# Kernel optimization log

Measured on AMD Instinct MI355X. Metric: run time of the kernel, lower is better.

## Reference

```python
import jax, jax.numpy as jnp
import numpy as np

B, T, E, H, A = 64, 1024, 512, 512, 512  # batch, src_len, enc_dim, hidden, attention_dim
D_IN = 512                                # decoder input embedding dim; cell input = D_IN + E


def setup_inputs() -> dict:
    key = jax.random.key(0)
    ks = jax.random.split(key, 10)
    s = 0.05  # small init to keep tanh/sigmoid unsaturated
    return {
        "inputs":  jax.random.normal(ks[0], (B, D_IN), jnp.float32),
        "states":  jax.random.normal(ks[1], (B, H), jnp.float32),
        "encoded": jax.random.normal(ks[2], (B, T, E), jnp.float32),
        "W_enc":   jax.random.normal(ks[3], (E, A), jnp.float32) * s,
        "W_state": jax.random.normal(ks[4], (H, A), jnp.float32) * s,
        "v":       jax.random.normal(ks[5], (A,), jnp.float32) * s,
        "W_ih":    jax.random.normal(ks[6], (3 * H, D_IN + E), jnp.float32) * s,
        "W_hh":    jax.random.normal(ks[7], (3 * H, H), jnp.float32) * s,
        "b_ih":    jnp.zeros((3 * H,), jnp.float32),
        "b_hh":    jnp.zeros((3 * H,), jnp.float32),
    }


def reference(inputs, states, encoded, W_enc, W_state, v, W_ih, W_hh, b_ih, b_hh):
    # --- Bahdanau additive attention (one decoder step) ---
    enc_proj = jnp.einsum("bte,ea->bta", encoded, W_enc)      # setup_memory projection
    st_proj = states @ W_state                                  # [B,A]
    scores = jnp.tanh(enc_proj + st_proj[:, None, :]) @ v       # [B,T]
    weights = jax.nn.softmax(scores, axis=-1)                   # [B,T]
    context = jnp.einsum("bt,bte->be", weights, encoded)       # [B,E]

    # --- GRU cell step on concat(inputs, context) (torch.nn.GRUCell math) ---
    x = jnp.concatenate([inputs, context], axis=-1)             # [B, D_IN+E]
    gi = x @ W_ih.T + b_ih                                      # [B, 3H]
    gh = states @ W_hh.T + b_hh                                 # [B, 3H]
    i_r, i_z, i_n = jnp.split(gi, 3, axis=-1)
    h_r, h_z, h_n = jnp.split(gh, 3, axis=-1)
    r = jax.nn.sigmoid(i_r + h_r)
    z = jax.nn.sigmoid(i_z + h_z)
    n = jnp.tanh(i_n + r * h_n)
    return (1.0 - z) * n + z * states                           # [B,H]
```

## Files before the change

kernel.cpp:

```cpp
#include <hip/hip_runtime.h>
#include <hip/hip_bf16.h>

#define BN   64
#define TN   1024
#define EN   512
#define AN   512
#define HN   512
#define G3H  1536

typedef __bf16 bf16x8 __attribute__((ext_vector_type(8)));
typedef __bf16 bf16x4 __attribute__((ext_vector_type(4)));
typedef float  f32x8  __attribute__((ext_vector_type(8)));
typedef float  f32x4  __attribute__((ext_vector_type(4)));
typedef unsigned int uint4v __attribute__((ext_vector_type(4)));

__device__ __forceinline__ float fast_tanh(float x) {
    float e = __expf(2.0f * x);
    return 1.0f - 2.0f / (e + 1.0f);
}
__device__ __forceinline__ float fast_sigmoid(float x) {
    return 1.0f / (1.0f + __expf(-x));
}

#define GL2LDS16(gsrc, ldst)                                                  \
    __builtin_amdgcn_global_load_lds(                                         \
        (const __attribute__((address_space(1))) unsigned int*)(gsrc),        \
        (__attribute__((address_space(3))) unsigned int*)(ldst), 16, 0, 0)

__global__ __launch_bounds__(256) void prep_kernel(
    const float* __restrict__ states, const float* __restrict__ W_enc,
    const float* __restrict__ W_state, const float* __restrict__ inputs,
    const float* __restrict__ W_ih, const float* __restrict__ W_hh,
    float* __restrict__ stp, __bf16* __restrict__ wencT,
    __bf16* __restrict__ xbf, __bf16* __restrict__ stbf,
    __bf16* __restrict__ wihbf, __bf16* __restrict__ whhbf,
    float* __restrict__ scores)
{
    __shared__ float srow[512];
    int blk = blockIdx.x, tid = threadIdx.x;

    if (blk < 64) {
        int b = blk;
        srow[tid] = states[b * 512 + tid];
        srow[tid + 256] = states[b * 512 + tid + 256];
        __syncthreads();
        int n0 = tid, n1 = tid + 256;
        float a0 = 0.f, a1 = 0.f;
        for (int k = 0; k < 512; ++k) {
            float s = srow[k];
            a0 += s * W_state[k * 512 + n0];
            a1 += s * W_state[k * 512 + n1];
        }
        stp[b * 512 + n0] = a0;
        stp[b * 512 + n1] = a1;
    } else if (blk < 72) {
        int n = (blk - 64) * 64 + (tid & 63);
        int cseg = tid >> 6;
        for (int c = cseg * 16; c < cseg * 16 + 16; ++c) {
            f32x8 f;
            #pragma unroll
            for (int j = 0; j < 8; ++j) f[j] = W_enc[(c * 8 + j) * 512 + n];
            int cs = (c & ~7) | ((c & 7) ^ (n & 7));
            *(bf16x8*)(wencT + n * 512 + cs * 8) = __builtin_convertvector(f, bf16x8);
        }
    } else if (blk < 840) {
        int base4 = (blk - 72) * 512 + tid * 2;
        #pragma unroll
        for (int j = 0; j < 2; ++j) {
            int i4 = base4 + j;
            f32x4 f = *(const f32x4*)(W_ih + i4 * 4);
            *(bf16x4*)(wihbf + i4 * 4) = __builtin_convertvector(f, bf16x4);
        }
    } else if (blk < 1224) {
        int base4 = (blk - 840) * 512 + tid * 2;
        #pragma unroll
        for (int j = 0; j < 2; ++j) {
            int i4 = base4 + j;
            f32x4 f = *(const f32x4*)(W_hh + i4 * 4);
            *(bf16x4*)(whhbf + i4 * 4) = __builtin_convertvector(f, bf16x4);
        }
    } else if (blk < 1240) {
        int base4 = (blk - 1224) * 512 + tid * 2;
        #pragma unroll
        for (int j = 0; j < 2; ++j) {
            int i4 = base4 + j;
            int e = i4 * 4;
            int b = e >> 9, c = e & 511;
            f32x4 f = *(const f32x4*)(inputs + e);
            *(bf16x4*)(xbf + b * 1024 + c) = __builtin_convertvector(f, bf16x4);
        }
    } else if (blk < 1256) {
        int base4 = (blk - 1240) * 512 + tid * 2;
        #pragma unroll
        for (int j = 0; j < 2; ++j) {
            int i4 = base4 + j;
            int e = i4 * 4;
            f32x4 f = *(const f32x4*)(states + e);
            *(bf16x4*)(stbf + e) = __builtin_convertvector(f, bf16x4);
        }
    } else {
        int e = (blk - 1256) * 1024 + tid * 4;
        *(f32x4*)(scores + e) = (f32x4){0.f, 0.f, 0.f, 0.f};
    }
}

__global__ __launch_bounds__(256) void cvt_kernel(
    const float* __restrict__ enc, __bf16* __restrict__ encbf)
{
    size_t row0 = (size_t)blockIdx.x * 8;
    int tid = threadIdx.x;
    #pragma unroll
    for (int i = 0; i < 2; ++i) {
        int p = i * 256 + tid;
        int r = p >> 6, c = p & 63;
        size_t row = row0 + r;
        f32x8 f = *(const f32x8*)(enc + row * 512 + c * 8);
        int cs = (c & ~7) | ((c & 7) ^ (int)(row & 7));
        *(bf16x8*)(encbf + row * 512 + cs * 8) = __builtin_convertvector(f, bf16x8);
    }
}

__global__ __launch_bounds__(256, 4) void score_kernel(
    const __bf16* __restrict__ encbf, const __bf16* __restrict__ wencT,
    const float* __restrict__ stp, const float* __restrict__ v,
    float* __restrict__ scores)
{
    __shared__ __align__(16) __bf16 As[128 * 64];
    __shared__ __align__(16) __bf16 Bs[128 * 64];
    __shared__ float sacc[256];

    int tid = threadIdx.x;
    int bid = blockIdx.x;
    int orig = (bid & 7) * 256 + (bid >> 3);
    int rt = orig >> 2, ct = orig & 3;
    int grow0 = rt * 128;
    int c0 = ct * 128;
    int b = grow0 >> 10;

    int lane = tid & 63, wid = tid >> 6;
    int wrow = wid >> 1, wcol = wid & 1;
    int l15 = lane & 15, g = lane >> 4;

    f32x4 acc[4][4];
    #pragma unroll
    for (int m = 0; m < 4; ++m)
        #pragma unroll
        for (int n = 0; n < 4; ++n) acc[m][n] = (f32x4){0.f, 0.f, 0.f, 0.f};

    for (int ks = 0; ks < 8; ++ks) {
        #pragma unroll
        for (int i = 0; i < 4; ++i) {
            int p = i * 256 + tid;
            int row = p >> 3, c = p & 7;
            const __bf16* src = encbf + (size_t)(grow0 + row) * 512 + ks * 64 + c * 8;
            char* dst = (char*)As + (i * 256 + wid * 64) * 16;
            GL2LDS16(src, dst);
        }
        #pragma unroll
        for (int i = 0; i < 4; ++i) {
            int p = i * 256 + tid;
            int row = p >> 3, c = p & 7;
            const __bf16* src = wencT + (size_t)(c0 + row) * 512 + ks * 64 + c * 8;
            char* dst = (char*)Bs + (i * 256 + wid * 64) * 16;
            GL2LDS16(src, dst);
        }
        __syncthreads();
        #pragma unroll
        for (int kk = 0; kk < 2; ++kk) {
            bf16x8 af[4], bfr[4];
            #pragma unroll
            for (int m = 0; m < 4; ++m) {
                int row = wrow * 64 + m * 16 + l15;
                int cch = (kk * 4 + g) ^ (row & 7);
                af[m] = *(const bf16x8*)((char*)As + row * 128 + cch * 16);
            }
            #pragma unroll
            for (int n = 0; n < 4; ++n) {
                int row = wcol * 64 + n * 16 + l15;
                int cch = (kk * 4 + g) ^ (row & 7);
                bfr[n] = *(const bf16x8*)((char*)Bs + row * 128 + cch * 16);
            }
            #pragma unroll
            for (int m = 0; m < 4; ++m)
                #pragma unroll
                for (int n = 0; n < 4; ++n)
                    acc[m][n] = __builtin_amdgcn_mfma_f32_16x16x32_bf16(
                        af[m], bfr[n], acc[m][n], 0, 0, 0);
        }
        if (ks < 7) __syncthreads();
    }

    float sv[4], vw[4];
    #pragma unroll
    for (int n = 0; n < 4; ++n) {
        int col = c0 + wcol * 64 + n * 16 + l15;
        sv[n] = stp[b * 512 + col];
        vw[n] = v[col];
    }
    float rp[16];
    #pragma unroll
    for (int i = 0; i < 16; ++i) rp[i] = 0.f;
    #pragma unroll
    for (int m = 0; m < 4; ++m)
        #pragma unroll
        for (int n = 0; n < 4; ++n) {
            #pragma unroll
            for (int r = 0; r < 4; ++r)
                rp[m * 4 + r] += vw[n] * fast_tanh(acc[m][n][r] + sv[n]);
        }
    #pragma unroll
    for (int i = 0; i < 16; ++i) {
        rp[i] += __shfl_xor(rp[i], 1);
        rp[i] += __shfl_xor(rp[i], 2);
        rp[i] += __shfl_xor(rp[i], 4);
        rp[i] += __shfl_xor(rp[i], 8);
    }
    if (l15 == 0) {
        #pragma unroll
        for (int m = 0; m < 4; ++m)
            #pragma unroll
            for (int r = 0; r < 4; ++r)
                sacc[wcol * 128 + wrow * 64 + m * 16 + g * 4 + r] = rp[m * 4 + r];
    }
    __syncthreads();
    if (tid < 128)
        atomicAdd(scores + grow0 + tid, sacc[tid] + sacc[128 + tid]);
}

__global__ __launch_bounds__(256) void ctx_kernel(
    const float* __restrict__ scores, const __bf16* __restrict__ encbf,
    __bf16* __restrict__ xbf)
{
    __shared__ float wsm[1024];
    __shared__ float red[4][128];
    __shared__ float tmp[8];
    int tid = threadIdx.x, lane = tid & 63, w = tid >> 6;
    int b = blockIdx.x >> 2, c0 = (blockIdx.x & 3) * 128;

    f32x4 s = *(const f32x4*)(scores + b * 1024 + tid * 4);
    float m = fmaxf(fmaxf(s[0], s[1]), fmaxf(s[2], s[3]));
    #pragma unroll
    for (int off = 32; off >= 1; off >>= 1) m = fmaxf(m, __shfl_xor(m, off));
    if (lane == 0) tmp[w] = m;
    __syncthreads();
    float M = fmaxf(fmaxf(tmp[0], tmp[1]), fmaxf(tmp[2], tmp[3]));
    float e0 = __expf(s[0] - M), e1 = __expf(s[1] - M);
    float e2 = __expf(s[2] - M), e3 = __expf(s[3] - M);
    wsm[tid * 4 + 0] = e0; wsm[tid * 4 + 1] = e1;
    wsm[tid * 4 + 2] = e2; wsm[tid * 4 + 3] = e3;
    float sum = e0 + e1 + e2 + e3;
    #pragma unroll
    for (int off = 32; off >= 1; off >>= 1) sum += __shfl_xor(sum, off);
    if (lane == 0) tmp[4 + w] = sum;
    __syncthreads();
    float S = tmp[4] + tmp[5] + tmp[6] + tmp[7];

    int q = lane >> 4, li = lane & 15;
    int ch0 = (c0 >> 3) + li;
    float a[8];
    #pragma unroll
    for (int k = 0; k < 8; ++k) a[k] = 0.f;
    const __bf16* ebase = encbf + (size_t)(b * 1024) * 512;
    for (int j = 0; j < 64; ++j) {
        int t = w * 256 + q + 4 * j;
        float wt = wsm[t];
        int chw = (ch0 & ~7) | ((ch0 & 7) ^ (t & 7));
        bf16x8 ev = *(const bf16x8*)(ebase + (size_t)t * 512 + chw * 8);
        #pragma unroll
        for (int k = 0; k < 8; ++k) a[k] += wt * (float)ev[k];
    }
    #pragma unroll
    for (int k = 0; k < 8; ++k) {
        a[k] += __shfl_xor(a[k], 16);
        a[k] += __shfl_xor(a[k], 32);
    }
    if (lane < 16) {
        #pragma unroll
        for (int k = 0; k < 8; ++k) red[w][li * 8 + k] = a[k];
    }
    __syncthreads();
    if (tid < 128) {
        float c = (red[0][tid] + red[1][tid] + red[2][tid] + red[3][tid]) / S;
        xbf[b * 1024 + 512 + c0 + tid] = (__bf16)c;
    }
}

__global__ __launch_bounds__(256) void gru_gemm(
    const __bf16* __restrict__ xbf, const __bf16* __restrict__ stbf,
    const __bf16* __restrict__ wihbf, const __bf16* __restrict__ whhbf,
    const float* __restrict__ b_ih, const float* __restrict__ b_hh,
    float* __restrict__ gi, float* __restrict__ gh)
{
    __shared__ __align__(16) __bf16 As[64 * 72];
    __shared__ __align__(16) __bf16 Bs[128 * 72];
    int blk = blockIdx.x, tid = threadIdx.x;
    bool is_gh = blk >= 12;
    int n0 = (is_gh ? blk - 12 : blk) * 128;
    int K = is_gh ? 512 : 1024;
    const __bf16* Aptr = is_gh ? stbf : xbf;
    const __bf16* Bptr = is_gh ? whhbf : wihbf;
    const float* bias = is_gh ? b_hh : b_ih;
    float* outp = is_gh ? gh : gi;

    int lane = tid & 63, wid = tid >> 6, l15 = lane & 15, g = lane >> 4;
    f32x4 acc[4][2];
    #pragma unroll
    for (int i = 0; i < 4; ++i)
        #pragma unroll
        for (int j = 0; j < 2; ++j) acc[i][j] = (f32x4){0.f, 0.f, 0.f, 0.f};

    int nkc = K >> 6;
    for (int kc = 0; kc < nkc; ++kc) {
        int k0 = kc * 64;
        #pragma unroll
        for (int q = 0; q < 2; ++q) {
            int ch = tid * 2 + q, row = ch >> 3, seg = ch & 7;
            uint4v u = *(const uint4v*)(Aptr + row * K + k0 + seg * 8);
            *(uint4v*)(As + row * 72 + seg * 8) = u;
        }
        #pragma unroll
        for (int q = 0; q < 4; ++q) {
            int ch = tid * 4 + q, row = ch >> 3, seg = ch & 7;
            uint4v u = *(const uint4v*)(Bptr + (n0 + row) * K + k0 + seg * 8);
            *(uint4v*)(Bs + row * 72 + seg * 8) = u;
        }
        __syncthreads();
        #pragma unroll
        for (int kk = 0; kk < 2; ++kk) {
            bf16x8 af[4], bfr[2];
            #pragma unroll
            for (int m = 0; m < 4; ++m)
                af[m] = *(const bf16x8*)(As + (m * 16 + l15) * 72 + kk * 32 + g * 8);
            #pragma unroll
            for (int n = 0; n < 2; ++n)
                bfr[n] = *(const bf16x8*)(Bs + (wid * 32 + n * 16 + l15) * 72 + kk * 32 + g * 8);
            #pragma unroll
            for (int m = 0; m < 4; ++m)
                #pragma unroll
                for (int n = 0; n < 2; ++n)
                    acc[m][n] = __builtin_amdgcn_mfma_f32_16x16x32_bf16(
                        af[m], bfr[n], acc[m][n], 0, 0, 0);
        }
        __syncthreads();
    }
    #pragma unroll
    for (int m = 0; m < 4; ++m)
        #pragma unroll
        for (int n = 0; n < 2; ++n) {
            int col = n0 + wid * 32 + n * 16 + l15;
            float bb = bias[col];
            #pragma unroll
            for (int r = 0; r < 4; ++r) {
                int brow = m * 16 + g * 4 + r;
                outp[brow * 1536 + col] = acc[m][n][r] + bb;
            }
        }
}

__global__ __launch_bounds__(256) void gru_gates(
    const float* __restrict__ gi, const float* __restrict__ gh,
    const float* __restrict__ states, float* __restrict__ out)
{
    int i = blockIdx.x * 256 + threadIdx.x;
    int b = i >> 9, j = i & 511;
    const float* gib = gi + b * 1536;
    const float* ghb = gh + b * 1536;
    float r = fast_sigmoid(gib[j] + ghb[j]);
    float z = fast_sigmoid(gib[512 + j] + ghb[512 + j]);
    float n = fast_tanh(gib[1024 + j] + r * ghb[1024 + j]);
    out[i] = (1.f - z) * n + z * states[i];
}

extern "C" void kernel_launch(void* const* d_in, const int* in_sizes, int n_in,
                              void* d_out, int out_size, void* d_ws, size_t ws_size,
                              hipStream_t stream)
{
    const float* inputs  = (const float*)d_in[0];
    const float* states  = (const float*)d_in[1];
    const float* encoded = (const float*)d_in[2];
    const float* W_enc   = (const float*)d_in[3];
    const float* W_state = (const float*)d_in[4];
    const float* v       = (const float*)d_in[5];
    const float* W_ih    = (const float*)d_in[6];
    const float* W_hh    = (const float*)d_in[7];
    const float* b_ih    = (const float*)d_in[8];
    const float* b_hh    = (const float*)d_in[9];
    float* out = (float*)d_out;
    char* ws = (char*)d_ws;

    float*  stp    = (float*)(ws + 0);
    __bf16* wencT  = (__bf16*)(ws + 131072);
    float*  scores = (float*)(ws + 655360);
    __bf16* xbf    = (__bf16*)(ws + 917504);
    __bf16* stbf   = (__bf16*)(ws + 1048576);
    __bf16* wihbf  = (__bf16*)(ws + 1114112);
    __bf16* whhbf  = (__bf16*)(ws + 4259840);
    float*  gi     = (float*)(ws + 5832704);
    float*  gh     = (float*)(ws + 6225920);
    __bf16* encbf  = (__bf16*)(ws + 6619136);

    prep_kernel<<<1320, 256, 0, stream>>>(states, W_enc, W_state, inputs, W_ih, W_hh,
                                          stp, wencT, xbf, stbf, wihbf, whhbf, scores);
    cvt_kernel<<<8192, 256, 0, stream>>>(encoded, encbf);
    score_kernel<<<2048, 256, 0, stream>>>(encbf, wencT, stp, v, scores);
    ctx_kernel<<<256, 256, 0, stream>>>(scores, encbf, xbf);
    gru_gemm<<<24, 256, 0, stream>>>(xbf, stbf, wihbf, whhbf, b_ih, b_hh, gi, gh);
    gru_gates<<<128, 256, 0, stream>>>(gi, gh, states, out);
}
```

Before: 140.5 us.

## Enlarge score GEMM tiles to 256x256 with double-buffered LDS prefetch

The score GEMM now uses 512-thread blocks computing 256x256 tiles (8x4 MFMA tiles per wave). It double-buffers the A and B K-slices in 128KB of dynamic LDS, issuing the next slice's global-to-LDS loads before computing the current one and waiting with explicit vmcnt. MFMA sections are wrapped in setprio. The goal is to hide load latency, raise data reuse per loaded byte, and cut the number of atomics. The cost is more registers, 128KB of LDS per block, which limits occupancy to one block per CU, and a dependence on the 160KB LDS limit. Only 512 blocks are launched.

```diff
diff --git a/kernel.cpp b/kernel.cpp
--- a/kernel.cpp
+++ b/kernel.cpp
@@ -120,74 +120,87 @@
     }
 }
 
-__global__ __launch_bounds__(256, 4) void score_kernel(
+__global__ __launch_bounds__(512, 2) void score_kernel(
     const __bf16* __restrict__ encbf, const __bf16* __restrict__ wencT,
     const float* __restrict__ stp, const float* __restrict__ v,
     float* __restrict__ scores)
 {
-    __shared__ __align__(16) __bf16 As[128 * 64];
-    __shared__ __align__(16) __bf16 Bs[128 * 64];
-    __shared__ float sacc[256];
-
+    extern __shared__ char smem[];
     int tid = threadIdx.x;
     int bid = blockIdx.x;
-    int orig = (bid & 7) * 256 + (bid >> 3);
-    int rt = orig >> 2, ct = orig & 3;
-    int grow0 = rt * 128;
-    int c0 = ct * 128;
+    int orig = (bid & 7) * 64 + (bid >> 3);
+    int rt = orig >> 1, ct = orig & 1;
+    int grow0 = rt * 256;
+    int c0 = ct * 256;
     int b = grow0 >> 10;
 
     int lane = tid & 63, wid = tid >> 6;
-    int wrow = wid >> 1, wcol = wid & 1;
+    int wrow = wid >> 2, wcol = wid & 3;
     int l15 = lane & 15, g = lane >> 4;
 
-    f32x4 acc[4][4];
-    #pragma unroll
-    for (int m = 0; m < 4; ++m)
+    f32x4 acc[8][4];
+    #pragma unroll
+    for (int m = 0; m < 8; ++m)
         #pragma unroll
         for (int n = 0; n < 4; ++n) acc[m][n] = (f32x4){0.f, 0.f, 0.f, 0.f};
 
-    for (int ks = 0; ks < 8; ++ks) {
+    auto issue = [&](int ks, int buf) {
+        char* Abase = smem + buf * 32768;
+        char* Bbase = smem + 65536 + buf * 32768;
         #pragma unroll
         for (int i = 0; i < 4; ++i) {
-            int p = i * 256 + tid;
+            int p = i * 512 + tid;
             int row = p >> 3, c = p & 7;
             const __bf16* src = encbf + (size_t)(grow0 + row) * 512 + ks * 64 + c * 8;
-            char* dst = (char*)As + (i * 256 + wid * 64) * 16;
-            GL2LDS16(src, dst);
+            GL2LDS16(src, Abase + (i * 512 + wid * 64) * 16);
         }
         #pragma unroll
         for (int i = 0; i < 4; ++i) {
-            int p = i * 256 + tid;
+            int p = i * 512 + tid;
             int row = p >> 3, c = p & 7;
             const __bf16* src = wencT + (size_t)(c0 + row) * 512 + ks * 64 + c * 8;
-            char* dst = (char*)Bs + (i * 256 + wid * 64) * 16;
-            GL2LDS16(src, dst);
-        }
-        __syncthreads();
+            GL2LDS16(src, Bbase + (i * 512 + wid * 64) * 16);
+        }
+    };
+
+    issue(0, 0);
+
+    #pragma unroll
+    for (int ks = 0; ks < 8; ++ks) {
+        if (ks < 7) {
+            issue(ks + 1, (ks + 1) & 1);
+            asm volatile("s_waitcnt vmcnt(8)" ::: "memory");
+        } else {
+            asm volatile("s_waitcnt vmcnt(0)" ::: "memory");
+        }
+        __builtin_amdgcn_s_barrier();
+        const char* Acur = smem + (ks & 1) * 32768;
+        const char* Bcur = smem + 65536 + (ks & 1) * 32768;
         #pragma unroll
         for (int kk = 0; kk < 2; ++kk) {
-            bf16x8 af[4], bfr[4];
-            #pragma unroll
-            for (int m = 0; m < 4; ++m) {
-                int row = wrow * 64 + m * 16 + l15;
+            bf16x8 af[8], bfr[4];
+            #pragma unroll
+            for (int m = 0; m < 8; ++m) {
+                int row = wrow * 128 + m * 16 + l15;
                 int cch = (kk * 4 + g) ^ (row & 7);
-                af[m] = *(const bf16x8*)((char*)As + row * 128 + cch * 16);
+                af[m] = *(const bf16x8*)(Acur + row * 128 + cch * 16);
             }
             #pragma unroll
             for (int n = 0; n < 4; ++n) {
                 int row = wcol * 64 + n * 16 + l15;
                 int cch = (kk * 4 + g) ^ (row & 7);
-                bfr[n] = *(const bf16x8*)((char*)Bs + row * 128 + cch * 16);
+                bfr[n] = *(const bf16x8*)(Bcur + row * 128 + cch * 16);
             }
-            #pragma unroll
-            for (int m = 0; m < 4; ++m)
+            __builtin_amdgcn_s_setprio(1);
+            #pragma unroll
+            for (int m = 0; m < 8; ++m)
                 #pragma unroll
                 for (int n = 0; n < 4; ++n)
                     acc[m][n] = __builtin_amdgcn_mfma_f32_16x16x32_bf16(
                         af[m], bfr[n], acc[m][n], 0, 0, 0);
-        }
-        if (ks < 7) __syncthreads();
+            __builtin_amdgcn_s_setprio(0);
+        }
+        __builtin_amdgcn_s_barrier();
     }
 
     float sv[4], vw[4];
@@ -197,11 +210,11 @@
         sv[n] = stp[b * 512 + col];
         vw[n] = v[col];
     }
-    float rp[16];
-    #pragma unroll
-    for (int i = 0; i < 16; ++i) rp[i] = 0.f;
-    #pragma unroll
-    for (int m = 0; m < 4; ++m)
+    float rp[32];
+    #pragma unroll
+    for (int i = 0; i < 32; ++i) rp[i] = 0.f;
+    #pragma unroll
+    for (int m = 0; m < 8; ++m)
         #pragma unroll
         for (int n = 0; n < 4; ++n) {
             #pragma unroll
@@ -209,22 +222,26 @@
                 rp[m * 4 + r] += vw[n] * fast_tanh(acc[m][n][r] + sv[n]);
         }
     #pragma unroll
-    for (int i = 0; i < 16; ++i) {
+    for (int i = 0; i < 32; ++i) {
         rp[i] += __shfl_xor(rp[i], 1);
         rp[i] += __shfl_xor(rp[i], 2);
         rp[i] += __shfl_xor(rp[i], 4);
         rp[i] += __shfl_xor(rp[i], 8);
     }
+    float* sacc = (float*)smem;
+    __syncthreads();
     if (l15 == 0) {
         #pragma unroll
-        for (int m = 0; m < 4; ++m)
+        for (int m = 0; m < 8; ++m)
             #pragma unroll
             for (int r = 0; r < 4; ++r)
-                sacc[wcol * 128 + wrow * 64 + m * 16 + g * 4 + r] = rp[m * 4 + r];
+                sacc[wcol * 256 + wrow * 128 + m * 16 + g * 4 + r] = rp[m * 4 + r];
     }
     __syncthreads();
-    if (tid < 128)
-        atomicAdd(scores + grow0 + tid, sacc[tid] + sacc[128 + tid]);
+    if (tid < 256) {
+        float val = sacc[tid] + sacc[256 + tid] + sacc[512 + tid] + sacc[768 + tid];
+        atomicAdd(scores + grow0 + tid, val);
+    }
 }
 
 __global__ __launch_bounds__(256) void ctx_kernel(
@@ -402,7 +419,7 @@
     prep_kernel<<<1320, 256, 0, stream>>>(states, W_enc, W_state, inputs, W_ih, W_hh,
                                           stp, wencT, xbf, stbf, wihbf, whhbf, scores);
     cvt_kernel<<<8192, 256, 0, stream>>>(encoded, encbf);
-    score_kernel<<<2048, 256, 0, stream>>>(encbf, wencT, stp, v, scores);
+    score_kernel<<<512, 512, 131072, stream>>>(encbf, wencT, stp, v, scores);
     ctx_kernel<<<256, 256, 0, stream>>>(scores, encbf, xbf);
     gru_gemm<<<24, 256, 0, stream>>>(xbf, stbf, wihbf, whhbf, b_ih, b_hh, gi, gh);
     gru_gates<<<128, 256, 0, stream>>>(gi, gh, states, out);
```

Result: no change. 138.1 us (-1.7%).
